# Kernel tuning notes

Measured on AMD Instinct MI355X. Metric: run time of the kernel, lower is better.

## Reference

```python
import jax, jax.numpy as jnp
import numpy as np

D_MODEL = 2048
NUM_HEADS = 16
D_FF = 8192
BATCH = 4
SEQ = 2048


def setup_inputs() -> dict:
    key = jax.random.key(0)
    ks = jax.random.split(key, 16)
    s_attn = 1.0 / np.sqrt(D_MODEL)
    s_ff1 = 1.0 / np.sqrt(D_MODEL)
    s_ff2 = 1.0 / np.sqrt(D_FF)
    return {
        "x": jax.random.normal(ks[0], (BATCH, SEQ, D_MODEL), dtype=jnp.float32),
        "Wq": jax.random.normal(ks[1], (D_MODEL, D_MODEL), dtype=jnp.float32) * s_attn,
        "bq": jnp.zeros((D_MODEL,), dtype=jnp.float32),
        "Wk": jax.random.normal(ks[2], (D_MODEL, D_MODEL), dtype=jnp.float32) * s_attn,
        "bk": jnp.zeros((D_MODEL,), dtype=jnp.float32),
        "Wv": jax.random.normal(ks[3], (D_MODEL, D_MODEL), dtype=jnp.float32) * s_attn,
        "bv": jnp.zeros((D_MODEL,), dtype=jnp.float32),
        "Wo": jax.random.normal(ks[4], (D_MODEL, D_MODEL), dtype=jnp.float32) * s_attn,
        "bo": jnp.zeros((D_MODEL,), dtype=jnp.float32),
        "W1": jax.random.normal(ks[5], (D_MODEL, D_FF), dtype=jnp.float32) * s_ff1,
        "b1": jnp.zeros((D_FF,), dtype=jnp.float32),
        "W2": jax.random.normal(ks[6], (D_FF, D_MODEL), dtype=jnp.float32) * s_ff2,
        "b2": jnp.zeros((D_MODEL,), dtype=jnp.float32),
        "ln1_g": jnp.ones((D_MODEL,), dtype=jnp.float32),
        "ln1_b": jnp.zeros((D_MODEL,), dtype=jnp.float32),
        "ln2_g": jnp.ones((D_MODEL,), dtype=jnp.float32),
        "ln2_b": jnp.zeros((D_MODEL,), dtype=jnp.float32),
    }


def _layer_norm(x, g, b, eps=1e-5):
    mu = jnp.mean(x, axis=-1, keepdims=True)
    var = jnp.mean(jnp.square(x - mu), axis=-1, keepdims=True)
    return (x - mu) * jax.lax.rsqrt(var + eps) * g + b


def _attention(h, Wq, bq, Wk, bk, Wv, bv, Wo, bo):
    B, S, D = h.shape
    H = NUM_HEADS
    dk = D // H
    q = (h @ Wq + bq).reshape(B, S, H, dk).transpose(0, 2, 1, 3)  # bhsd
    k = (h @ Wk + bk).reshape(B, S, H, dk).transpose(0, 2, 1, 3)
    v = (h @ Wv + bv).reshape(B, S, H, dk).transpose(0, 2, 1, 3)
    logits = jnp.einsum("bhqd,bhkd->bhqk", q, k) / jnp.sqrt(jnp.float32(dk))
    causal = jnp.triu(jnp.ones((S, S), dtype=bool), k=1)  # True above diagonal
    logits = jnp.where(causal, -jnp.inf, logits)
    attn = jax.nn.softmax(logits, axis=-1)
    out = jnp.einsum("bhqk,bhkd->bhqd", attn, v)
    out = out.transpose(0, 2, 1, 3).reshape(B, S, D)
    return out @ Wo + bo


def reference(x, Wq, bq, Wk, bk, Wv, bv, Wo, bo, W1, b1, W2, b2,
              ln1_g, ln1_b, ln2_g, ln2_b):
    # Pre-LN attention block + residual
    h = _layer_norm(x, ln1_g, ln1_b)
    x = x + _attention(h, Wq, bq, Wk, bk, Wv, bv, Wo, bo)
    # Pre-LN FFN block + residual (GELU activation)
    h = _layer_norm(x, ln2_g, ln2_b)
    ff = jax.nn.gelu(h @ W1 + b1, approximate=False) @ W2 + b2
    return x + ff
```

## Files before the change

kernel.cpp:

```cpp
#include <hip/hip_runtime.h>
#include <hip/hip_bf16.h>

#define D_MODEL 2048
#define NUM_HEADS 16
#define D_FF 8192
#define BATCH 4
#define SEQ 2048
#define DK 128
#define MTOT (BATCH * SEQ)

typedef __attribute__((ext_vector_type(8))) short short8;
typedef __attribute__((ext_vector_type(4))) short short4v;
typedef __attribute__((ext_vector_type(4))) float f32x4;

#define MFMA16(a, b, c) __builtin_amdgcn_mfma_f32_16x16x32_bf16(a, b, c, 0, 0, 0)

#define GLOAD16(gp, lp)                                                        \
  __builtin_amdgcn_global_load_lds(                                            \
      (const __attribute__((address_space(1))) void*)(gp),                     \
      (__attribute__((address_space(3))) void*)(lp), 16, 0, 0)

static __device__ __forceinline__ unsigned short f2bf(float f) {
  return __builtin_bit_cast(unsigned short, __float2bfloat16(f));
}

__global__ __launch_bounds__(256) void transpose_cvt_kernel(
    const float* __restrict__ in, __hip_bfloat16* __restrict__ out, int K, int N) {
  __shared__ float tile[32][33];
  const int n0 = blockIdx.x * 32, k0 = blockIdx.y * 32;
  const int tx = threadIdx.x & 31, ty = threadIdx.x >> 5;
#pragma unroll
  for (int i = 0; i < 4; ++i)
    tile[ty + i * 8][tx] = in[(size_t)(k0 + ty + i * 8) * N + n0 + tx];
  __syncthreads();
#pragma unroll
  for (int i = 0; i < 4; ++i)
    out[(size_t)(n0 + ty + i * 8) * K + k0 + tx] = __float2bfloat16(tile[tx][ty + i * 8]);
}

__global__ __launch_bounds__(256) void layernorm_kernel(
    const float* __restrict__ x, const float* __restrict__ g,
    const float* __restrict__ bta, __hip_bfloat16* __restrict__ out) {
  const int row = blockIdx.x;
  const int tid = threadIdx.x;
  const float* xr = x + (size_t)row * D_MODEL;
  float4 v0 = *(const float4*)(xr + tid * 8);
  float4 v1 = *(const float4*)(xr + tid * 8 + 4);
  float s = v0.x + v0.y + v0.z + v0.w + v1.x + v1.y + v1.z + v1.w;
  float q = v0.x * v0.x + v0.y * v0.y + v0.z * v0.z + v0.w * v0.w +
            v1.x * v1.x + v1.y * v1.y + v1.z * v1.z + v1.w * v1.w;
#pragma unroll
  for (int off = 1; off < 64; off <<= 1) {
    s += __shfl_xor(s, off);
    q += __shfl_xor(q, off);
  }
  __shared__ float rs[4], rq[4];
  if ((tid & 63) == 0) {
    rs[tid >> 6] = s;
    rq[tid >> 6] = q;
  }
  __syncthreads();
  s = rs[0] + rs[1] + rs[2] + rs[3];
  q = rq[0] + rq[1] + rq[2] + rq[3];
  const float mu = s * (1.0f / D_MODEL);
  const float var = q * (1.0f / D_MODEL) - mu * mu;
  const float rstd = rsqrtf(var + 1e-5f);
  float4 g0 = *(const float4*)(g + tid * 8);
  float4 g1 = *(const float4*)(g + tid * 8 + 4);
  float4 b0 = *(const float4*)(bta + tid * 8);
  float4 b1 = *(const float4*)(bta + tid * 8 + 4);
  short8 o;
  o[0] = (short)f2bf((v0.x - mu) * rstd * g0.x + b0.x);
  o[1] = (short)f2bf((v0.y - mu) * rstd * g0.y + b0.y);
  o[2] = (short)f2bf((v0.z - mu) * rstd * g0.z + b0.z);
  o[3] = (short)f2bf((v0.w - mu) * rstd * g0.w + b0.w);
  o[4] = (short)f2bf((v1.x - mu) * rstd * g1.x + b1.x);
  o[5] = (short)f2bf((v1.y - mu) * rstd * g1.y + b1.y);
  o[6] = (short)f2bf((v1.z - mu) * rstd * g1.z + b1.z);
  o[7] = (short)f2bf((v1.w - mu) * rstd * g1.w + b1.w);
  *(short8*)(out + (size_t)row * D_MODEL + tid * 8) = o;
}

enum { EPI_BF16 = 0, EPI_VT = 1, EPI_RESID = 2, EPI_GELU = 3 };

template <int EPI>
__global__ __launch_bounds__(512, 2) void gemm_kernel(
    const __hip_bfloat16* __restrict__ A, const __hip_bfloat16* __restrict__ Bt,
    const float* __restrict__ bias, const float* __restrict__ resid,
    void* __restrict__ outv, int M, int N, int K) {
  __shared__ __align__(16) unsigned char lds[3][49152];
  const int tid = threadIdx.x;
  const int lane = tid & 63, w = tid >> 6;
  const int l15 = lane & 15, lg = lane >> 4;
  const int m0 = blockIdx.y * 256, n0 = blockIdx.x * 128;
  const int wm = (w >> 1) * 64, wn = (w & 1) * 64;

  f32x4 acc[4][4] = {};

  const int row8 = lane >> 3;
  const int g8 = (lane & 7) ^ row8;

  auto STAGE = [&](int tt) {
    unsigned char* db = lds[tt % 3];
    const size_t ko = (size_t)tt * 64;
#pragma unroll
    for (int i = 0; i < 4; ++i) {
      const int c = w * 4 + i;
      const int row = c * 8 + row8;
      GLOAD16(A + (size_t)(m0 + row) * K + ko + g8 * 8, db + c * 1024);
    }
#pragma unroll
    for (int i = 0; i < 2; ++i) {
      const int c = w * 2 + i;
      const int row = c * 8 + row8;
      GLOAD16(Bt + (size_t)(n0 + row) * K + ko + g8 * 8, db + 32768 + c * 1024);
    }
  };
  auto COMPUTE = [&](int tt) {
    const unsigned char* db = lds[tt % 3];
#pragma unroll
    for (int ks = 0; ks < 2; ++ks) {
      const int cb = ks * 4 + lg;
      short8 af[4], bf[4];
#pragma unroll
      for (int f = 0; f < 4; ++f) {
        const int ra = wm + f * 16 + l15;
        af[f] = *(const short8*)(db + ra * 128 + ((cb ^ (ra & 7)) << 4));
        const int rb = wn + f * 16 + l15;
        bf[f] = *(const short8*)(db + 32768 + rb * 128 + ((cb ^ (rb & 7)) << 4));
      }
      __builtin_amdgcn_s_setprio(1);
#pragma unroll
      for (int fi = 0; fi < 4; ++fi)
#pragma unroll
        for (int fj = 0; fj < 4; ++fj)
          acc[fi][fj] = MFMA16(af[fi], bf[fj], acc[fi][fj]);
      __builtin_amdgcn_s_setprio(0);
    }
  };

  const int nt = K >> 6;
  STAGE(0);
  STAGE(1);
  for (int t = 0; t < nt; ++t) {
    if (t + 2 < nt) {
      asm volatile("s_waitcnt vmcnt(6)" ::: "memory");
      __builtin_amdgcn_s_barrier();
      STAGE(t + 2);
    } else if (t + 2 == nt) {
      asm volatile("s_waitcnt vmcnt(6)" ::: "memory");
      __builtin_amdgcn_s_barrier();
    } else {
      asm volatile("s_waitcnt vmcnt(0)" ::: "memory");
      __builtin_amdgcn_s_barrier();
    }
    COMPUTE(t);
  }

#pragma unroll
  for (int fi = 0; fi < 4; ++fi) {
#pragma unroll
    for (int fj = 0; fj < 4; ++fj) {
      const int mb = m0 + wm + fi * 16 + lg * 4;
      const int n = n0 + wn + fj * 16 + l15;
      const float bv = bias ? bias[n] : 0.0f;
      if constexpr (EPI == EPI_VT) {
        const int bb = mb >> 11, ss = mb & (SEQ - 1);
        const int hh = n >> 7, dd = n & (DK - 1);
        short4v pk;
#pragma unroll
        for (int r = 0; r < 4; ++r) pk[r] = (short)f2bf(acc[fi][fj][r] + bv);
        __hip_bfloat16* o = (__hip_bfloat16*)outv;
        *(short4v*)(o + ((size_t)((bb * NUM_HEADS + hh) * DK + dd)) * SEQ + ss) = pk;
      } else {
#pragma unroll
        for (int r = 0; r < 4; ++r) {
          const int m = mb + r;
          const float v = acc[fi][fj][r] + bv;
          if constexpr (EPI == EPI_BF16) {
            ((__hip_bfloat16*)outv)[(size_t)m * N + n] = __float2bfloat16(v);
          } else if constexpr (EPI == EPI_GELU) {
            const float ge = 0.5f * v * (1.0f + erff(v * 0.70710678118654752f));
            ((__hip_bfloat16*)outv)[(size_t)m * N + n] = __float2bfloat16(ge);
          } else {
            ((float*)outv)[(size_t)m * N + n] = resid[(size_t)m * N + n] + v;
          }
        }
      }
    }
  }
}

__global__ __launch_bounds__(512, 4) void attn_kernel(
    const __hip_bfloat16* __restrict__ Qm, const __hip_bfloat16* __restrict__ Km,
    const __hip_bfloat16* __restrict__ Vt, __hip_bfloat16* __restrict__ Om) {
  __shared__ __align__(16) unsigned char Kl[2][16384];
  __shared__ __align__(16) unsigned char Vl[2][16384];
  __shared__ __align__(16) unsigned char Pl[16384];
  const int tid = threadIdx.x;
  const int lane = tid & 63, w = tid >> 6;
  const int l15 = lane & 15, lg = lane >> 4;
  const int bh = blockIdx.y, b = bh >> 4, h = bh & 15;
  const int q0 = ((int)gridDim.x - 1 - (int)blockIdx.x) * 128;
  const int qw = q0 + w * 16;
  const int row8 = lane >> 3;
  const int nt = (q0 >> 6) + 2;

  short8 qf[4];
  const __hip_bfloat16* qbase = Qm + (size_t)(b * SEQ + qw + l15) * D_MODEL + h * DK;
#pragma unroll
  for (int ks = 0; ks < 4; ++ks) qf[ks] = *(const short8*)(qbase + ks * 32 + lg * 8);

  float m_run[4], l_run[4];
  f32x4 acc_o[8];
#pragma unroll
  for (int r = 0; r < 4; ++r) { m_run[r] = -1e30f; l_run[r] = 0.0f; }
#pragma unroll
  for (int fd = 0; fd < 8; ++fd) acc_o[fd] = (f32x4){0.f, 0.f, 0.f, 0.f};

  auto STAGE = [&](int tt) {
    unsigned char* kb = Kl[tt & 1];
    unsigned char* vb = Vl[tt & 1];
    const int t0 = tt * 64;
#pragma unroll
    for (int i = 0; i < 2; ++i) {
      const int c = w * 2 + i;
      const int row = c * 4 + lg;
      const int gcb = l15 ^ (row & 7);
      GLOAD16(Km + (size_t)(b * SEQ + t0 + row) * D_MODEL + h * DK + gcb * 8,
              kb + c * 1024);
    }
#pragma unroll
    for (int i = 0; i < 2; ++i) {
      const int c = w * 2 + i;
      const int row = c * 8 + row8;
      const int gcb = (lane & 7) ^ (row & 7);
      GLOAD16(Vt + (size_t)(bh * DK + row) * SEQ + t0 + gcb * 8, vb + c * 1024);
    }
  };

  STAGE(0);
  for (int t = 0; t < nt; ++t) {
    const int t0 = t * 64;
    if (t + 1 < nt) {
      STAGE(t + 1);
      asm volatile("s_waitcnt vmcnt(4)" ::: "memory");
    } else {
      asm volatile("s_waitcnt vmcnt(0)" ::: "memory");
    }
    __builtin_amdgcn_s_barrier();
    asm volatile("" ::: "memory");
    if (t0 <= qw + 15) {
      const unsigned char* kb = Kl[t & 1];
      const unsigned char* vb = Vl[t & 1];
      f32x4 sacc[4];
#pragma unroll
      for (int fn = 0; fn < 4; ++fn) sacc[fn] = (f32x4){0.f, 0.f, 0.f, 0.f};
      __builtin_amdgcn_s_setprio(1);
#pragma unroll
      for (int ks = 0; ks < 4; ++ks) {
        const int cb = ks * 4 + lg;
#pragma unroll
        for (int fn = 0; fn < 4; ++fn) {
          const int rn = fn * 16 + l15;
          short8 kf = *(const short8*)(kb + rn * 256 + ((cb ^ (rn & 7)) << 4));
          sacc[fn] = MFMA16(qf[ks], kf, sacc[fn]);
        }
      }
      __builtin_amdgcn_s_setprio(0);
      const float scale = 0.088388347648318447f;
      float mt[4] = {-1e30f, -1e30f, -1e30f, -1e30f};
#pragma unroll
      for (int fn = 0; fn < 4; ++fn) {
        const int key = t0 + fn * 16 + l15;
#pragma unroll
        for (int r = 0; r < 4; ++r) {
          const int qg = qw + lg * 4 + r;
          float sv = sacc[fn][r] * scale;
          sv = (key <= qg) ? sv : -1e30f;
          sacc[fn][r] = sv;
          mt[r] = fmaxf(mt[r], sv);
        }
      }
#pragma unroll
      for (int r = 0; r < 4; ++r)
#pragma unroll
        for (int off = 1; off < 16; off <<= 1) mt[r] = fmaxf(mt[r], __shfl_xor(mt[r], off));
      int ok = 1;
#pragma unroll
      for (int r = 0; r < 4; ++r) ok = ok && (mt[r] <= m_run[r] + 8.0f);
      const bool defer = __all(ok);
      float alpha[4];
      if (!defer) {
#pragma unroll
        for (int r = 0; r < 4; ++r) {
          const float mnew = fmaxf(m_run[r], mt[r]);
          alpha[r] = __expf(m_run[r] - mnew);
          m_run[r] = mnew;
        }
      }
      float ls[4] = {0.f, 0.f, 0.f, 0.f};
#pragma unroll
      for (int fn = 0; fn < 4; ++fn)
#pragma unroll
        for (int r = 0; r < 4; ++r) {
          const float p = __expf(sacc[fn][r] - m_run[r]);
          sacc[fn][r] = p;
          ls[r] += p;
        }
#pragma unroll
      for (int r = 0; r < 4; ++r) {
#pragma unroll
        for (int off = 1; off < 16; off <<= 1) ls[r] += __shfl_xor(ls[r], off);
        l_run[r] = (defer ? l_run[r] : l_run[r] * alpha[r]) + ls[r];
      }
      if (!defer) {
#pragma unroll
        for (int fd = 0; fd < 8; ++fd)
#pragma unroll
          for (int r = 0; r < 4; ++r) acc_o[fd][r] *= alpha[r];
      }
      unsigned char* pw = Pl + w * 2048;
#pragma unroll
      for (int fn = 0; fn < 4; ++fn) {
        const int tt = fn * 16 + l15;
#pragma unroll
        for (int r = 0; r < 4; ++r) {
          const int qq = lg * 4 + r;
          *(unsigned short*)(pw + qq * 128 + (((tt >> 3) ^ (qq & 7)) << 4) +
                             (tt & 7) * 2) = f2bf(sacc[fn][r]);
        }
      }
#pragma unroll
      for (int ks = 0; ks < 2; ++ks) {
        const int tb = ks * 4 + lg;
        short8 pf = *(const short8*)(Pl + w * 2048 + l15 * 128 +
                                     ((tb ^ (l15 & 7)) << 4));
        const int cb = ks * 4 + lg;
        __builtin_amdgcn_s_setprio(1);
#pragma unroll
        for (int fd = 0; fd < 8; ++fd) {
          const int rv = fd * 16 + l15;
          short8 vf = *(const short8*)(vb + rv * 128 + ((cb ^ (rv & 7)) << 4));
          acc_o[fd] = MFMA16(pf, vf, acc_o[fd]);
        }
        __builtin_amdgcn_s_setprio(0);
      }
    }
    asm volatile("" ::: "memory");
    __builtin_amdgcn_s_barrier();
    asm volatile("" ::: "memory");
  }
#pragma unroll
  for (int r = 0; r < 4; ++r) {
    const float inv = 1.0f / l_run[r];
    const int qg = qw + lg * 4 + r;
    __hip_bfloat16* ob = Om + (size_t)(b * SEQ + qg) * D_MODEL + h * DK + l15;
#pragma unroll
    for (int fd = 0; fd < 8; ++fd)
      ob[fd * 16] = __float2bfloat16(acc_o[fd][r] * inv);
  }
}

extern "C" void kernel_launch(void* const* d_in, const int* in_sizes, int n_in,
                              void* d_out, int out_size, void* d_ws, size_t ws_size,
                              hipStream_t stream) {
  (void)in_sizes; (void)n_in; (void)out_size;
  const size_t MB = 1024 * 1024;
  if (ws_size < 192 * MB) return;

  const float* x  = (const float*)d_in[0];
  const float* Wq = (const float*)d_in[1];
  const float* bq = (const float*)d_in[2];
  const float* Wk = (const float*)d_in[3];
  const float* bk = (const float*)d_in[4];
  const float* Wv = (const float*)d_in[5];
  const float* bv = (const float*)d_in[6];
  const float* Wo = (const float*)d_in[7];
  const float* bo = (const float*)d_in[8];
  const float* W1 = (const float*)d_in[9];
  const float* b1 = (const float*)d_in[10];
  const float* W2 = (const float*)d_in[11];
  const float* b2 = (const float*)d_in[12];
  const float* g1 = (const float*)d_in[13];
  const float* be1 = (const float*)d_in[14];
  const float* g2 = (const float*)d_in[15];
  const float* be2 = (const float*)d_in[16];

  char* ws = (char*)d_ws;
  __hip_bfloat16* Hb  = (__hip_bfloat16*)(ws + 0 * MB);
  __hip_bfloat16* Qb  = (__hip_bfloat16*)(ws + 32 * MB);
  __hip_bfloat16* Kb  = (__hip_bfloat16*)(ws + 64 * MB);
  __hip_bfloat16* Vtb = (__hip_bfloat16*)(ws + 96 * MB);
  __hip_bfloat16* AOb = (__hip_bfloat16*)(ws + 128 * MB);
  __hip_bfloat16* W1T = (__hip_bfloat16*)(ws + 32 * MB);
  __hip_bfloat16* W2T = (__hip_bfloat16*)(ws + 64 * MB);
  __hip_bfloat16* FF1 = (__hip_bfloat16*)(ws + 96 * MB);
  __hip_bfloat16* WqT = (__hip_bfloat16*)(ws + 160 * MB);
  __hip_bfloat16* WkT = (__hip_bfloat16*)(ws + 168 * MB);
  __hip_bfloat16* WvT = (__hip_bfloat16*)(ws + 176 * MB);
  __hip_bfloat16* WoT = (__hip_bfloat16*)(ws + 184 * MB);
  float* X2 = (float*)d_out;

  const dim3 tb(256);
  transpose_cvt_kernel<<<dim3(64, 64), tb, 0, stream>>>(Wq, WqT, 2048, 2048);
  transpose_cvt_kernel<<<dim3(64, 64), tb, 0, stream>>>(Wk, WkT, 2048, 2048);
  transpose_cvt_kernel<<<dim3(64, 64), tb, 0, stream>>>(Wv, WvT, 2048, 2048);
  transpose_cvt_kernel<<<dim3(64, 64), tb, 0, stream>>>(Wo, WoT, 2048, 2048);

  layernorm_kernel<<<MTOT, tb, 0, stream>>>(x, g1, be1, Hb);

  const dim3 gQKV(2048 / 128, MTOT / 256);
  gemm_kernel<EPI_BF16><<<gQKV, 512, 0, stream>>>(Hb, WqT, bq, nullptr, Qb, MTOT, 2048, 2048);
  gemm_kernel<EPI_BF16><<<gQKV, 512, 0, stream>>>(Hb, WkT, bk, nullptr, Kb, MTOT, 2048, 2048);
  gemm_kernel<EPI_VT><<<gQKV, 512, 0, stream>>>(Hb, WvT, bv, nullptr, Vtb, MTOT, 2048, 2048);

  attn_kernel<<<dim3(SEQ / 128, BATCH * NUM_HEADS), dim3(512), 0, stream>>>(Qb, Kb, Vtb, AOb);

  transpose_cvt_kernel<<<dim3(256, 64), tb, 0, stream>>>(W1, W1T, 2048, 8192);
  transpose_cvt_kernel<<<dim3(64, 256), tb, 0, stream>>>(W2, W2T, 8192, 2048);

  gemm_kernel<EPI_RESID><<<gQKV, 512, 0, stream>>>(AOb, WoT, bo, x, X2, MTOT, 2048, 2048);

  layernorm_kernel<<<MTOT, tb, 0, stream>>>(X2, g2, be2, Hb);

  for (int c = 0; c < 2; ++c) {
    const size_t moff = (size_t)c * 4096;
    gemm_kernel<EPI_GELU><<<dim3(8192 / 128, 4096 / 256), 512, 0, stream>>>(
        Hb + moff * D_MODEL, W1T, b1, nullptr, FF1, 4096, 8192, 2048);
    gemm_kernel<EPI_RESID><<<dim3(2048 / 128, 4096 / 256), 512, 0, stream>>>(
        FF1, W2T, b2, X2 + moff * D_MODEL, X2 + moff * D_MODEL, 4096, 2048, 8192);
  }
}
```

Measured before the change: 1.328 ms.

## Enlarge GEMM tiles to 256x256, swizzle block order, unchunk FFN GEMMs

The GEMM tile grows from 256x128 to 256x256, with each wave computing 128x64, to raise arithmetic intensity. The LDS pipeline drops from three stages to two and adds a second barrier per iteration. Block indices are remapped into groups of 8 row tiles for L2 locality. The two-chunk FFN split is replaced by full-M launches with W1T and W2T reusing one workspace slot, and the attention P-tile LDS swizzle changes to a rotation pattern to cut bank conflicts. The larger tile doubles accumulator registers (128 floats per lane), which may cost occupancy or cause spills, and the shallower pipeline hides less memory latency.

```diff
diff --git a/kernel.cpp b/kernel.cpp
--- a/kernel.cpp
+++ b/kernel.cpp
@@ -87,21 +87,25 @@
 __global__ __launch_bounds__(512, 2) void gemm_kernel(
     const __hip_bfloat16* __restrict__ A, const __hip_bfloat16* __restrict__ Bt,
     const float* __restrict__ bias, const float* __restrict__ resid,
-    void* __restrict__ outv, int M, int N, int K) {
-  __shared__ __align__(16) unsigned char lds[3][49152];
+    void* __restrict__ outv, int M, int N, int K, int nbx) {
+  __shared__ __align__(16) unsigned char lds[2][65536];
   const int tid = threadIdx.x;
   const int lane = tid & 63, w = tid >> 6;
   const int l15 = lane & 15, lg = lane >> 4;
-  const int m0 = blockIdx.y * 256, n0 = blockIdx.x * 128;
-  const int wm = (w >> 1) * 64, wn = (w & 1) * 64;
-
-  f32x4 acc[4][4] = {};
+  const int d = blockIdx.x;
+  const int qd = d >> 3;
+  const int cC = qd % nbx;
+  const int rC = (qd / nbx) * 8 + (d & 7);
+  const int m0 = rC * 256, n0 = cC * 256;
+  const int wm = (w >> 2) * 128, wn = (w & 3) * 64;
+
+  f32x4 acc[8][4] = {};
 
   const int row8 = lane >> 3;
   const int g8 = (lane & 7) ^ row8;
 
   auto STAGE = [&](int tt) {
-    unsigned char* db = lds[tt % 3];
+    unsigned char* db = lds[tt & 1];
     const size_t ko = (size_t)tt * 64;
 #pragma unroll
     for (int i = 0; i < 4; ++i) {
@@ -110,28 +114,31 @@
       GLOAD16(A + (size_t)(m0 + row) * K + ko + g8 * 8, db + c * 1024);
     }
 #pragma unroll
-    for (int i = 0; i < 2; ++i) {
-      const int c = w * 2 + i;
+    for (int i = 0; i < 4; ++i) {
+      const int c = w * 4 + i;
       const int row = c * 8 + row8;
       GLOAD16(Bt + (size_t)(n0 + row) * K + ko + g8 * 8, db + 32768 + c * 1024);
     }
   };
   auto COMPUTE = [&](int tt) {
-    const unsigned char* db = lds[tt % 3];
+    const unsigned char* db = lds[tt & 1];
 #pragma unroll
     for (int ks = 0; ks < 2; ++ks) {
       const int cb = ks * 4 + lg;
-      short8 af[4], bf[4];
-#pragma unroll
-      for (int f = 0; f < 4; ++f) {
+      short8 af[8], bf[4];
+#pragma unroll
+      for (int f = 0; f < 8; ++f) {
         const int ra = wm + f * 16 + l15;
         af[f] = *(const short8*)(db + ra * 128 + ((cb ^ (ra & 7)) << 4));
+      }
+#pragma unroll
+      for (int f = 0; f < 4; ++f) {
         const int rb = wn + f * 16 + l15;
         bf[f] = *(const short8*)(db + 32768 + rb * 128 + ((cb ^ (rb & 7)) << 4));
       }
       __builtin_amdgcn_s_setprio(1);
 #pragma unroll
-      for (int fi = 0; fi < 4; ++fi)
+      for (int fi = 0; fi < 8; ++fi)
 #pragma unroll
         for (int fj = 0; fj < 4; ++fj)
           acc[fi][fj] = MFMA16(af[fi], bf[fj], acc[fi][fj]);
@@ -143,22 +150,19 @@
   STAGE(0);
   STAGE(1);
   for (int t = 0; t < nt; ++t) {
-    if (t + 2 < nt) {
-      asm volatile("s_waitcnt vmcnt(6)" ::: "memory");
-      __builtin_amdgcn_s_barrier();
-      STAGE(t + 2);
-    } else if (t + 2 == nt) {
-      asm volatile("s_waitcnt vmcnt(6)" ::: "memory");
-      __builtin_amdgcn_s_barrier();
-    } else {
+    if (t < nt - 1)
+      asm volatile("s_waitcnt vmcnt(8)" ::: "memory");
+    else
       asm volatile("s_waitcnt vmcnt(0)" ::: "memory");
-      __builtin_amdgcn_s_barrier();
-    }
+    __builtin_amdgcn_s_barrier();
     COMPUTE(t);
-  }
-
-#pragma unroll
-  for (int fi = 0; fi < 4; ++fi) {
+    asm volatile("" ::: "memory");
+    __builtin_amdgcn_s_barrier();
+    if (t + 2 < nt) STAGE(t + 2);
+  }
+
+#pragma unroll
+  for (int fi = 0; fi < 8; ++fi) {
 #pragma unroll
     for (int fj = 0; fj < 4; ++fj) {
       const int mb = m0 + wm + fi * 16 + lg * 4;
@@ -327,7 +331,8 @@
 #pragma unroll
         for (int r = 0; r < 4; ++r) {
           const int qq = lg * 4 + r;
-          *(unsigned short*)(pw + qq * 128 + (((tt >> 3) ^ (qq & 7)) << 4) +
+          *(unsigned short*)(pw + qq * 128 +
+                             ((((tt >> 3) + qq + (qq >> 3)) & 7) << 4) +
                              (tt & 7) * 2) = f2bf(sacc[fn][r]);
         }
       }
@@ -335,7 +340,7 @@
       for (int ks = 0; ks < 2; ++ks) {
         const int tb = ks * 4 + lg;
         short8 pf = *(const short8*)(Pl + w * 2048 + l15 * 128 +
-                                     ((tb ^ (l15 & 7)) << 4));
+                                     (((tb + l15 + (l15 >> 3)) & 7) << 4));
         const int cb = ks * 4 + lg;
         __builtin_amdgcn_s_setprio(1);
 #pragma unroll
@@ -393,13 +398,13 @@
   __hip_bfloat16* Kb  = (__hip_bfloat16*)(ws + 64 * MB);
   __hip_bfloat16* Vtb = (__hip_bfloat16*)(ws + 96 * MB);
   __hip_bfloat16* AOb = (__hip_bfloat16*)(ws + 128 * MB);
-  __hip_bfloat16* W1T = (__hip_bfloat16*)(ws + 32 * MB);
-  __hip_bfloat16* W2T = (__hip_bfloat16*)(ws + 64 * MB);
-  __hip_bfloat16* FF1 = (__hip_bfloat16*)(ws + 96 * MB);
+  __hip_bfloat16* FF1 = (__hip_bfloat16*)(ws + 32 * MB);
   __hip_bfloat16* WqT = (__hip_bfloat16*)(ws + 160 * MB);
   __hip_bfloat16* WkT = (__hip_bfloat16*)(ws + 168 * MB);
   __hip_bfloat16* WvT = (__hip_bfloat16*)(ws + 176 * MB);
   __hip_bfloat16* WoT = (__hip_bfloat16*)(ws + 184 * MB);
+  __hip_bfloat16* W1T = (__hip_bfloat16*)(ws + 160 * MB);
+  __hip_bfloat16* W2T = (__hip_bfloat16*)(ws + 160 * MB);
   float* X2 = (float*)d_out;
 
   const dim3 tb(256);
@@ -410,25 +415,18 @@
 
   layernorm_kernel<<<MTOT, tb, 0, stream>>>(x, g1, be1, Hb);
 
-  const dim3 gQKV(2048 / 128, MTOT / 256);
-  gemm_kernel<EPI_BF16><<<gQKV, 512, 0, stream>>>(Hb, WqT, bq, nullptr, Qb, MTOT, 2048, 2048);
-  gemm_kernel<EPI_BF16><<<gQKV, 512, 0, stream>>>(Hb, WkT, bk, nullptr, Kb, MTOT, 2048, 2048);
-  gemm_kernel<EPI_VT><<<gQKV, 512, 0, stream>>>(Hb, WvT, bv, nullptr, Vtb, MTOT, 2048, 2048);
+  gemm_kernel<EPI_BF16><<<256, 512, 0, stream>>>(Hb, WqT, bq, nullptr, Qb, MTOT, 2048, 2048, 8);
+  gemm_kernel<EPI_BF16><<<256, 512, 0, stream>>>(Hb, WkT, bk, nullptr, Kb, MTOT, 2048, 2048, 8);
+  gemm_kernel<EPI_VT><<<256, 512, 0, stream>>>(Hb, WvT, bv, nullptr, Vtb, MTOT, 2048, 2048, 8);
 
   attn_kernel<<<dim3(SEQ / 128, BATCH * NUM_HEADS), dim3(512), 0, stream>>>(Qb, Kb, Vtb, AOb);
 
+  gemm_kernel<EPI_RESID><<<256, 512, 0, stream>>>(AOb, WoT, bo, x, X2, MTOT, 2048, 2048, 8);
+
+  layernorm_kernel<<<MTOT, tb, 0, stream>>>(X2, g2, be2, Hb);
+
   transpose_cvt_kernel<<<dim3(256, 64), tb, 0, stream>>>(W1, W1T, 2048, 8192);
+  gemm_kernel<EPI_GELU><<<1024, 512, 0, stream>>>(Hb, W1T, b1, nullptr, FF1, MTOT, 8192, 2048, 32);
   transpose_cvt_kernel<<<dim3(64, 256), tb, 0, stream>>>(W2, W2T, 8192, 2048);
-
-  gemm_kernel<EPI_RESID><<<gQKV, 512, 0, stream>>>(AOb, WoT, bo, x, X2, MTOT, 2048, 2048);
-
-  layernorm_kernel<<<MTOT, tb, 0, stream>>>(X2, g2, be2, Hb);
-
-  for (int c = 0; c < 2; ++c) {
-    const size_t moff = (size_t)c * 4096;
-    gemm_kernel<EPI_GELU><<<dim3(8192 / 128, 4096 / 256), 512, 0, stream>>>(
-        Hb + moff * D_MODEL, W1T, b1, nullptr, FF1, 4096, 8192, 2048);
-    gemm_kernel<EPI_RESID><<<dim3(2048 / 128, 4096 / 256), 512, 0, stream>>>(
-        FF1, W2T, b2, X2 + moff * D_MODEL, X2 + moff * D_MODEL, 4096, 2048, 8192);
-  }
-}
+  gemm_kernel<EPI_RESID><<<256, 512, 0, stream>>>(FF1, W2T, b2, X2, X2, MTOT, 2048, 8192, 8);
+}
```

After: 1.274 ms. 1.04x faster.
